# Optimization experiments

Measured on AMD Instinct MI355X. Metric: run time of the kernel, lower is better.

Reference implementation:

```python
import jax, jax.numpy as jnp
import numpy as np

NEG_INF = -1e9  # same masked_fill constant as the torch module
ALPHA = 0.1     # LeakyReLU negative slope


def setup_inputs() -> dict:
    key = jax.random.key(0)
    k1, k2, k3, k4, k5 = jax.random.split(key, 5)
    B, N, Din, Dout = 8, 2048, 512, 512
    features = jax.random.normal(k1, (B, N, Din), dtype=jnp.float32)
    graph = jax.random.randint(k2, (B, N, N), 0, 2, dtype=jnp.int64)
    # xavier_uniform with gain=1.414: limit = gain*sqrt(6/(fan_in+fan_out))
    lim_w = 1.414 * np.sqrt(6.0 / (Din + Dout))
    w = jax.random.uniform(k3, (Din, Dout), jnp.float32, -lim_w, lim_w)
    lim_a = 1.414 * np.sqrt(6.0 / (Dout + 1))
    a1 = jax.random.uniform(k4, (Dout, 1), jnp.float32, -lim_a, lim_a)
    a2 = jax.random.uniform(k5, (Dout, 1), jnp.float32, -lim_a, lim_a)
    return {"features": features, "graph": graph, "w": w, "a1": a1, "a2": a2}


def reference(features, graph, w, a1, a2):
    # hidden: [B, N, Dout]
    hidden = jnp.einsum("bni,io->bno", features, w)
    s1 = hidden @ a1  # [B, N, 1] -> broadcasts over columns
    s2 = hidden @ a2  # [B, N, 1] -> transposed broadcasts over rows
    # e[b,i,j] = leaky_relu(s1[b,i] + s2[b,j])
    e = jax.nn.leaky_relu(s1 + jnp.swapaxes(s2, 1, 2), negative_slope=ALPHA)
    e = jnp.where(graph == 0, NEG_INF, e)
    attn = jax.nn.softmax(e, axis=-1)  # [B, N, N]; dropout p=0 -> identity
    h_prime = jnp.einsum("bij,bjo->bio", attn, hidden)
    return jax.nn.elu(h_prime)  # concat=True
```

## Files before the change

kernel.cpp:

```cpp
#include <hip/hip_runtime.h>
#include <math.h>

#define B_ 8
#define N_ 2048
#define D_ 512
#define NROWS (B_ * N_)
#define NEG_ALPHA 0.1f

typedef __bf16 bf16;
typedef __bf16 bf16x4 __attribute__((ext_vector_type(4)));
typedef __bf16 bf16x8 __attribute__((ext_vector_type(8)));
typedef float f32x4 __attribute__((ext_vector_type(4)));
typedef float f32x16 __attribute__((ext_vector_type(16)));

#define HTB_BATCH ((D_ / 32) * (N_ / 16) * 512)

__global__ __launch_bounds__(256) void k_prep(const float* __restrict__ W,
                                              bf16* __restrict__ Wt) {
  const int dout = blockIdx.x;
  const int t = threadIdx.x;
#pragma unroll
  for (int p = 0; p < 2; ++p) {
    int din = t + p * 256;
    Wt[dout * D_ + din] = (bf16)W[din * D_ + dout];
  }
}

__global__ __launch_bounds__(256) void k_wa(const float* __restrict__ W,
                                            const float* __restrict__ a1,
                                            const float* __restrict__ a2,
                                            float* __restrict__ wa1,
                                            float* __restrict__ wa2) {
  const int wv = threadIdx.x >> 6, lane = threadIdx.x & 63;
  const int row = blockIdx.x * 4 + wv;
  const float* wr = W + (size_t)row * D_;
  float d1 = 0.f, d2 = 0.f;
#pragma unroll
  for (int p = 0; p < 8; ++p) {
    int c = lane + p * 64;
    float w = wr[c];
    d1 = fmaf(w, a1[c], d1);
    d2 = fmaf(w, a2[c], d2);
  }
#pragma unroll
  for (int off = 32; off > 0; off >>= 1) {
    d1 += __shfl_down(d1, off, 64);
    d2 += __shfl_down(d2, off, 64);
  }
  if (lane == 0) {
    wa1[row] = d1;
    wa2[row] = d2;
  }
}

__global__ __launch_bounds__(256) void k_scores_x(const float* __restrict__ X,
                                                  const float* __restrict__ wa1,
                                                  const float* __restrict__ wa2,
                                                  float* __restrict__ s1,
                                                  float* __restrict__ s2) {
  const int wv = threadIdx.x >> 6, lane = threadIdx.x & 63;
  const int r = blockIdx.x * 4 + wv;
  const float* x = X + (size_t)r * D_;
  float d1 = 0.f, d2 = 0.f;
#pragma unroll
  for (int p = 0; p < 2; ++p) {
    int c = lane * 4 + p * 256;
    float4 xv = *(const float4*)&x[c];
    float4 w1 = *(const float4*)&wa1[c];
    float4 w2 = *(const float4*)&wa2[c];
    d1 += xv.x * w1.x + xv.y * w1.y + xv.z * w1.z + xv.w * w1.w;
    d2 += xv.x * w2.x + xv.y * w2.y + xv.z * w2.z + xv.w * w2.w;
  }
#pragma unroll
  for (int off = 32; off > 0; off >>= 1) {
    d1 += __shfl_down(d1, off, 64);
    d2 += __shfl_down(d2, off, 64);
  }
  if (lane == 0) {
    s1[r] = d1;
    s2[r] = d2;
  }
}

#define LDH 40

__global__ __launch_bounds__(256, 2) void k_hiddenT(const float* __restrict__ X,
                                                    const bf16* __restrict__ Wt,
                                                    bf16* __restrict__ HtB) {
  __shared__ bf16 As[128][LDH];
  __shared__ bf16 Bs[128][LDH];
  const int t = threadIdx.x;
  const int m0 = blockIdx.y * 128;
  const int n0 = blockIdx.x * 128;
  const int lane = t & 63, w = t >> 6;
  const int wm = w >> 1, wn = w & 1;
  const int l15 = lane & 15, q = lane >> 4;

  f32x4 acc[4][4];
#pragma unroll
  for (int i = 0; i < 4; ++i)
#pragma unroll
    for (int j = 0; j < 4; ++j) acc[i][j] = (f32x4){0.f, 0.f, 0.f, 0.f};

  bf16x8 av[2];
  float4 bv[4];
#pragma unroll
  for (int p = 0; p < 2; ++p) {
    int s = t + p * 256;
    av[p] = *(const bf16x8*)&Wt[(size_t)(m0 + (s >> 2)) * D_ + (s & 3) * 8];
  }
#pragma unroll
  for (int p = 0; p < 4; ++p) {
    int s = t + p * 256;
    bv[p] = *(const float4*)&X[(size_t)(n0 + (s >> 3)) * D_ + (s & 7) * 4];
  }

  for (int k0 = 0; k0 < D_; k0 += 32) {
    __syncthreads();
#pragma unroll
    for (int p = 0; p < 2; ++p) {
      int s = t + p * 256;
      *(bf16x8*)&As[s >> 2][(s & 3) * 8] = av[p];
    }
#pragma unroll
    for (int p = 0; p < 4; ++p) {
      int s = t + p * 256;
      float4 v = bv[p];
      bf16x4 h = {(bf16)v.x, (bf16)v.y, (bf16)v.z, (bf16)v.w};
      *(bf16x4*)&Bs[s >> 3][(s & 7) * 4] = h;
    }
    __syncthreads();
    if (k0 + 32 < D_) {
#pragma unroll
      for (int p = 0; p < 2; ++p) {
        int s = t + p * 256;
        av[p] = *(const bf16x8*)&Wt[(size_t)(m0 + (s >> 2)) * D_ + k0 + 32 + (s & 3) * 8];
      }
#pragma unroll
      for (int p = 0; p < 4; ++p) {
        int s = t + p * 256;
        bv[p] = *(const float4*)&X[(size_t)(n0 + (s >> 3)) * D_ + k0 + 32 + (s & 7) * 4];
      }
    }
    bf16x8 a[4], bb[4];
#pragma unroll
    for (int i = 0; i < 4; ++i)
      a[i] = *(const bf16x8*)&As[wm * 64 + i * 16 + l15][q * 8];
#pragma unroll
    for (int j = 0; j < 4; ++j)
      bb[j] = *(const bf16x8*)&Bs[wn * 64 + j * 16 + l15][q * 8];
#pragma unroll
    for (int i = 0; i < 4; ++i)
#pragma unroll
      for (int j = 0; j < 4; ++j)
        acc[i][j] =
            __builtin_amdgcn_mfma_f32_16x16x32_bf16(a[i], bb[j], acc[i][j], 0, 0, 0);
  }
#pragma unroll
  for (int i = 0; i < 4; ++i)
#pragma unroll
    for (int r = 0; r < 4; ++r) {
      int dout = m0 + wm * 64 + i * 16 + q * 4 + r;
#pragma unroll
      for (int j = 0; j < 4; ++j) {
        int row = n0 + wn * 64 + j * 16 + l15;
        int bb_ = row >> 11;
        int jj = row & (N_ - 1);
        size_t addr = (size_t)bb_ * HTB_BATCH +
                      ((size_t)((dout >> 5) * (N_ / 16) + (jj >> 4)) * 64 +
                       ((jj >> 3) & 1) * 32 + (dout & 31)) *
                          8 +
                      (jj & 7);
        HtB[addr] = (bf16)acc[i][j][r];
      }
    }
}

#define AT_BM 64
#define AT_BK 64
#define LDP 72
#define NIT (N_ / AT_BK)

#define ATTN_BODY(PS, BC, BN, G0, G1, IT)                                      \
  {                                                                            \
    const int j0_ = (IT)*AT_BK;                                                \
    int gg[8] = {G0.x, G0.y, G0.z, G0.w, G1.x, G1.y, G1.z, G1.w};              \
    {           \
      int itn = (IT) + 2;                                                      \
      int jg = (itn < NIT) ? itn * AT_BK : 0;                                  \
      G0 = *(const int4*)&Gb[(size_t)pi * N_ + jg + pj];                       \
      G1 = *(const int4*)&Gb[(size_t)pi * N_ + jg + pj + 4];                   \
    }                                                                          \
    float pv[8];                                                               \
    {                                                                          \
      f32x4 sA = *(const f32x4*)&s2s[j0_ + pj];                                \
      f32x4 sB = *(const f32x4*)&s2s[j0_ + pj + 4];                            \
      float sv[8] = {sA.x, sA.y, sA.z, sA.w, sB.x, sB.y, sB.z, sB.w};          \
      _Pragma("unroll") for (int q_ = 0; q_ < 8; ++q_) {                       \
        float e = s1r + sv[q_];                                                \
        e = (e > 0.f) ? e : NEG_ALPHA * e;                                     \
        pv[q_] = (gg[q_] != 0) ? __expf(e) : 0.f;                              \
        rsum += pv[q_];                                                        \
      }                                                                        \
    }                                                                          \
    {                                                                          \
      bf16x8 pb = {(bf16)pv[0], (bf16)pv[1], (bf16)pv[2], (bf16)pv[3],         \
                   (bf16)pv[4], (bf16)pv[5], (bf16)pv[6], (bf16)pv[7]};        \
      *(bf16x8*)&Ps[PS][pi][pj] = pb;                                          \
    }                                                                          \
    __syncthreads();            \
    {               \
      int j0n = ((IT) + 1 < NIT) ? ((IT) + 1) * AT_BK : 0;                     \
      _Pragma("unroll") for (int nt = 0; nt < 2; ++nt)                         \
          _Pragma("unroll") for (int ks = 0; ks < 4; ++ks)                     \
              BN[nt][ks] = *(const bf16x8*)&Hb[(size_t)((                      \
                  ((w * 2 + nt) * (N_ / 16) + (j0n >> 4) + ks) * 64 + lane))   \
                  * 8];                                                        \
    }                                                                          \
    _Pragma("unroll") for (int ks = 0; ks < 4; ++ks) {                         \
      const int ko = ks * 16 + hf * 8;                                         \
      bf16x8 a0 = *(const bf16x8*)&Ps[PS][r31][ko];                            \
      bf16x8 a1 = *(const bf16x8*)&Ps[PS][32 + r31][ko];                       \
      acc[0][0] = __builtin_amdgcn_mfma_f32_32x32x16_bf16(a0, BC[0][ks],       \
                                                          acc[0][0], 0, 0, 0); \
      acc[0][1] = __builtin_amdgcn_mfma_f32_32x32x16_bf16(a0, BC[1][ks],       \
                                                          acc[0][1], 0, 0, 0); \
      acc[1][0] = __builtin_amdgcn_mfma_f32_32x32x16_bf16(a1, BC[0][ks],       \
                                                          acc[1][0], 0, 0, 0); \
      acc[1][1] = __builtin_amdgcn_mfma_f32_32x32x16_bf16(a1, BC[1][ks],       \
                                                          acc[1][1], 0, 0, 0); \
    }                                                                          \
  }

__global__ __launch_bounds__(512) void k_attn(const bf16* __restrict__ HtB,
                                              const int* __restrict__ graph,
                                              const float* __restrict__ s1,
                                              const float* __restrict__ s2,
                                              float* __restrict__ out) {
  __shared__ __align__(16) bf16 Ps[2][AT_BM][LDP];
  __shared__ float s2s[N_];
  __shared__ float sum_part[AT_BM][8];
  __shared__ float row_sum[AT_BM];

  const int t = threadIdx.x;
  const int bid = blockIdx.x;
  const int b = bid & 7;
  const int i0 = (bid >> 3) * AT_BM;
  const int lane = t & 63, w = t >> 6;
  const int r31 = lane & 31, hf = lane >> 5;

  const bf16* Hb = HtB + (size_t)b * HTB_BATCH;
  const int* Gb = graph + ((size_t)b * N_ + i0) * N_;

  for (int c = t; c < N_; c += 512) s2s[c] = s2[b * N_ + c];

  const int pi = t >> 3;
  const int pj = (t & 7) * 8;
  const float s1r = s1[b * N_ + i0 + pi];
  float rsum = 0.f;

  f32x16 acc[2][2];
#pragma unroll
  for (int i = 0; i < 2; ++i)
#pragma unroll
    for (int j = 0; j < 2; ++j)
#pragma unroll
      for (int r = 0; r < 16; ++r) acc[i][j][r] = 0.f;

  bf16x8 bA[2][4], bB[2][4];
#pragma unroll
  for (int nt = 0; nt < 2; ++nt)
#pragma unroll
    for (int ks = 0; ks < 4; ++ks)
      bA[nt][ks] = *(const bf16x8*)&Hb[(size_t)(
          ((w * 2 + nt) * (N_ / 16) + ks) * 64 + lane) * 8];
  int4 ga0 = *(const int4*)&Gb[(size_t)pi * N_ + pj];
  int4 ga1 = *(const int4*)&Gb[(size_t)pi * N_ + pj + 4];
  int4 gb0 = *(const int4*)&Gb[(size_t)pi * N_ + AT_BK + pj];
  int4 gb1 = *(const int4*)&Gb[(size_t)pi * N_ + AT_BK + pj + 4];

  __syncthreads();

#pragma unroll 1
  for (int i2 = 0; i2 < NIT / 2; ++i2) {
    const int it0 = i2 * 2;
    ATTN_BODY(0, bA, bB, ga0, ga1, it0);
    ATTN_BODY(1, bB, bA, gb0, gb1, it0 + 1);
  }

  sum_part[pi][t & 7] = rsum;
  __syncthreads();
  if (t < AT_BM) {
    float s = 0.f;
#pragma unroll
    for (int k = 0; k < 8; ++k) s += sum_part[t][k];
    row_sum[t] = s;
  }
  __syncthreads();

#pragma unroll
  for (int mt = 0; mt < 2; ++mt) {
    float inv[16];
#pragma unroll
    for (int r = 0; r < 16; ++r)
      inv[r] = 1.f / row_sum[mt * 32 + (r & 3) + 8 * (r >> 2) + 4 * hf];
#pragma unroll
    for (int nt = 0; nt < 2; ++nt) {
      const int d = w * 64 + nt * 32 + r31;
#pragma unroll
      for (int r = 0; r < 16; ++r) {
        int i = mt * 32 + (r & 3) + 8 * (r >> 2) + 4 * hf;
        float x = acc[mt][nt][r] * inv[r];
        out[((size_t)b * N_ + i0 + i) * D_ + d] = (x > 0.f) ? x : expm1f(x);
      }
    }
  }
}

extern "C" void kernel_launch(void* const* d_in, const int* in_sizes, int n_in,
                              void* d_out, int out_size, void* d_ws,
                              size_t ws_size, hipStream_t stream) {
  const float* X = (const float*)d_in[0];
  const int* graph = (const int*)d_in[1];
  const float* W = (const float*)d_in[2];
  const float* a1 = (const float*)d_in[3];
  const float* a2 = (const float*)d_in[4];
  float* out = (float*)d_out;

  char* ws = (char*)d_ws;
  bf16* Wt = (bf16*)ws;
  bf16* HtB = (bf16*)(ws + (1 << 19));
  float* s1 = (float*)(ws + (1 << 19) + (16 << 20));
  float* s2 = s1 + NROWS;
  float* wa1 = s2 + NROWS;
  float* wa2 = wa1 + D_;

  hipLaunchKernelGGL(k_prep, dim3(512), dim3(256), 0, stream, W, Wt);
  hipLaunchKernelGGL(k_wa, dim3(128), dim3(256), 0, stream, W, a1, a2, wa1, wa2);
  hipLaunchKernelGGL(k_scores_x, dim3(NROWS / 4), dim3(256), 0, stream, X, wa1,
                     wa2, s1, s2);
  hipLaunchKernelGGL(k_hiddenT, dim3(NROWS / 128, D_ / 128), dim3(256), 0,
                     stream, X, Wt, HtB);
  hipLaunchKernelGGL(k_attn, dim3(N_ / AT_BM * B_), dim3(512), 0, stream, HtB,
                     graph, s1, s2, out);
}
```

Measured before the change: 276.6 us.

## Pre-pack adjacency mask to bits and stage it in LDS for attention

```diff
diff --git a/kernel.cpp b/kernel.cpp
--- a/kernel.cpp
+++ b/kernel.cpp
@@ -17,12 +17,22 @@
 
 __global__ __launch_bounds__(256) void k_prep(const float* __restrict__ W,
                                               bf16* __restrict__ Wt) {
-  const int dout = blockIdx.x;
-  const int t = threadIdx.x;
-#pragma unroll
-  for (int p = 0; p < 2; ++p) {
-    int din = t + p * 256;
-    Wt[dout * D_ + din] = (bf16)W[din * D_ + dout];
+  __shared__ float tile[64][65];
+  const int din0 = blockIdx.y * 64, dout0 = blockIdx.x * 64;
+  const int tx = threadIdx.x & 63, tg = threadIdx.x >> 6;
+#pragma unroll
+  for (int rr = 0; rr < 16; ++rr) {
+    int dr = tg * 16 + rr;
+    tile[dr][tx] = W[(size_t)(din0 + dr) * D_ + dout0 + tx];
+  }
+  __syncthreads();
+#pragma unroll
+  for (int rr = 0; rr < 4; ++rr) {
+    int dl = rr * 16 + (threadIdx.x >> 4);
+    int nl = (threadIdx.x & 15) * 4;
+    bf16x4 v = {(bf16)tile[nl][dl], (bf16)tile[nl + 1][dl],
+                (bf16)tile[nl + 2][dl], (bf16)tile[nl + 3][dl]};
+    *(bf16x4*)&Wt[(size_t)(dout0 + dl) * D_ + din0 + nl] = v;
   }
 }
 
@@ -57,7 +67,8 @@
                                                   const float* __restrict__ wa1,
                                                   const float* __restrict__ wa2,
                                                   float* __restrict__ s1,
-                                                  float* __restrict__ s2) {
+                                                  float* __restrict__ s2,
+                                                  bf16* __restrict__ Xb) {
   const int wv = threadIdx.x >> 6, lane = threadIdx.x & 63;
   const int r = blockIdx.x * 4 + wv;
   const float* x = X + (size_t)r * D_;
@@ -70,6 +81,8 @@
     float4 w2 = *(const float4*)&wa2[c];
     d1 += xv.x * w1.x + xv.y * w1.y + xv.z * w1.z + xv.w * w1.w;
     d2 += xv.x * w2.x + xv.y * w2.y + xv.z * w2.z + xv.w * w2.w;
+    bf16x4 h = {(bf16)xv.x, (bf16)xv.y, (bf16)xv.z, (bf16)xv.w};
+    *(bf16x4*)&Xb[(size_t)r * D_ + c] = h;
   }
 #pragma unroll
   for (int off = 32; off > 0; off >>= 1) {
@@ -82,9 +95,25 @@
   }
 }
 
+__global__ __launch_bounds__(256) void k_gpack(const int* __restrict__ G,
+                                               unsigned int* __restrict__ GB) {
+  const size_t g = (size_t)blockIdx.x * 256 + threadIdx.x;
+  const int* src = G + g * 32;
+  unsigned int bits = 0;
+#pragma unroll
+  for (int p = 0; p < 8; ++p) {
+    int4 v = *(const int4*)&src[p * 4];
+    bits |= (unsigned)(v.x != 0) << (p * 4);
+    bits |= (unsigned)(v.y != 0) << (p * 4 + 1);
+    bits |= (unsigned)(v.z != 0) << (p * 4 + 2);
+    bits |= (unsigned)(v.w != 0) << (p * 4 + 3);
+  }
+  GB[g] = bits;
+}
+
 #define LDH 40
 
-__global__ __launch_bounds__(256, 2) void k_hiddenT(const float* __restrict__ X,
+__global__ __launch_bounds__(256, 2) void k_hiddenT(const bf16* __restrict__ Xb,
                                                     const bf16* __restrict__ Wt,
                                                     bf16* __restrict__ HtB) {
   __shared__ bf16 As[128][LDH];
@@ -102,17 +131,12 @@
 #pragma unroll
     for (int j = 0; j < 4; ++j) acc[i][j] = (f32x4){0.f, 0.f, 0.f, 0.f};
 
-  bf16x8 av[2];
-  float4 bv[4];
+  bf16x8 av[2], bv[2];
 #pragma unroll
   for (int p = 0; p < 2; ++p) {
     int s = t + p * 256;
     av[p] = *(const bf16x8*)&Wt[(size_t)(m0 + (s >> 2)) * D_ + (s & 3) * 8];
-  }
-#pragma unroll
-  for (int p = 0; p < 4; ++p) {
-    int s = t + p * 256;
-    bv[p] = *(const float4*)&X[(size_t)(n0 + (s >> 3)) * D_ + (s & 7) * 4];
+    bv[p] = *(const bf16x8*)&Xb[(size_t)(n0 + (s >> 2)) * D_ + (s & 3) * 8];
   }
 
   for (int k0 = 0; k0 < D_; k0 += 32) {
@@ -121,13 +145,7 @@
     for (int p = 0; p < 2; ++p) {
       int s = t + p * 256;
       *(bf16x8*)&As[s >> 2][(s & 3) * 8] = av[p];
-    }
-#pragma unroll
-    for (int p = 0; p < 4; ++p) {
-      int s = t + p * 256;
-      float4 v = bv[p];
-      bf16x4 h = {(bf16)v.x, (bf16)v.y, (bf16)v.z, (bf16)v.w};
-      *(bf16x4*)&Bs[s >> 3][(s & 7) * 4] = h;
+      *(bf16x8*)&Bs[s >> 2][(s & 3) * 8] = bv[p];
     }
     __syncthreads();
     if (k0 + 32 < D_) {
@@ -135,11 +153,7 @@
       for (int p = 0; p < 2; ++p) {
         int s = t + p * 256;
         av[p] = *(const bf16x8*)&Wt[(size_t)(m0 + (s >> 2)) * D_ + k0 + 32 + (s & 3) * 8];
-      }
-#pragma unroll
-      for (int p = 0; p < 4; ++p) {
-        int s = t + p * 256;
-        bv[p] = *(const float4*)&X[(size_t)(n0 + (s >> 3)) * D_ + k0 + 32 + (s & 7) * 4];
+        bv[p] = *(const bf16x8*)&Xb[(size_t)(n0 + (s >> 2)) * D_ + k0 + 32 + (s & 3) * 8];
       }
     }
     bf16x8 a[4], bb[4];
@@ -180,17 +194,12 @@
 #define AT_BK 64
 #define LDP 72
 #define NIT (N_ / AT_BK)
-
-#define ATTN_BODY(PS, BC, BN, G0, G1, IT)                                      \
+#define GROW 272
+
+#define ATTN_BODY(PS, BC, BN, IT)                                              \
   {                                                                            \
     const int j0_ = (IT)*AT_BK;                                                \
-    int gg[8] = {G0.x, G0.y, G0.z, G0.w, G1.x, G1.y, G1.z, G1.w};              \
-    {           \
-      int itn = (IT) + 2;                                                      \
-      int jg = (itn < NIT) ? itn * AT_BK : 0;                                  \
-      G0 = *(const int4*)&Gb[(size_t)pi * N_ + jg + pj];                       \
-      G1 = *(const int4*)&Gb[(size_t)pi * N_ + jg + pj + 4];                   \
-    }                                                                          \
+    unsigned gbyte = gb_s[pi][(IT)*8 + (t & 7)];                               \
     float pv[8];                                                               \
     {                                                                          \
       f32x4 sA = *(const f32x4*)&s2s[j0_ + pj];                                \
@@ -199,7 +208,7 @@
       _Pragma("unroll") for (int q_ = 0; q_ < 8; ++q_) {                       \
         float e = s1r + sv[q_];                                                \
         e = (e > 0.f) ? e : NEG_ALPHA * e;                                     \
-        pv[q_] = (gg[q_] != 0) ? __expf(e) : 0.f;                              \
+        pv[q_] = ((gbyte >> q_) & 1) ? __expf(e) : 0.f;                        \
         rsum += pv[q_];                                                        \
       }                                                                        \
     }                                                                          \
@@ -233,12 +242,13 @@
   }
 
 __global__ __launch_bounds__(512) void k_attn(const bf16* __restrict__ HtB,
-                                              const int* __restrict__ graph,
+                                              const unsigned char* __restrict__ GB,
                                               const float* __restrict__ s1,
                                               const float* __restrict__ s2,
                                               float* __restrict__ out) {
   __shared__ __align__(16) bf16 Ps[2][AT_BM][LDP];
   __shared__ float s2s[N_];
+  __shared__ __align__(16) unsigned char gb_s[AT_BM][GROW];
   __shared__ float sum_part[AT_BM][8];
   __shared__ float row_sum[AT_BM];
 
@@ -250,9 +260,16 @@
   const int r31 = lane & 31, hf = lane >> 5;
 
   const bf16* Hb = HtB + (size_t)b * HTB_BATCH;
-  const int* Gb = graph + ((size_t)b * N_ + i0) * N_;
+  const unsigned char* GBb = GB + ((size_t)b * N_ + i0) * (N_ / 8);
 
   for (int c = t; c < N_; c += 512) s2s[c] = s2[b * N_ + c];
+  {
+    int gr = t >> 3, gc = (t & 7) * 32;
+    int4 w0 = *(const int4*)&GBb[(size_t)gr * (N_ / 8) + gc];
+    int4 w1 = *(const int4*)&GBb[(size_t)gr * (N_ / 8) + gc + 16];
+    *(int4*)&gb_s[gr][gc] = w0;
+    *(int4*)&gb_s[gr][gc + 16] = w1;
+  }
 
   const int pi = t >> 3;
   const int pj = (t & 7) * 8;
@@ -274,18 +291,14 @@
     for (int ks = 0; ks < 4; ++ks)
       bA[nt][ks] = *(const bf16x8*)&Hb[(size_t)(
           ((w * 2 + nt) * (N_ / 16) + ks) * 64 + lane) * 8];
-  int4 ga0 = *(const int4*)&Gb[(size_t)pi * N_ + pj];
-  int4 ga1 = *(const int4*)&Gb[(size_t)pi * N_ + pj + 4];
-  int4 gb0 = *(const int4*)&Gb[(size_t)pi * N_ + AT_BK + pj];
-  int4 gb1 = *(const int4*)&Gb[(size_t)pi * N_ + AT_BK + pj + 4];
 
   __syncthreads();
 
 #pragma unroll 1
   for (int i2 = 0; i2 < NIT / 2; ++i2) {
     const int it0 = i2 * 2;
-    ATTN_BODY(0, bA, bB, ga0, ga1, it0);
-    ATTN_BODY(1, bB, bA, gb0, gb1, it0 + 1);
+    ATTN_BODY(0, bA, bB, it0);
+    ATTN_BODY(1, bB, bA, it0 + 1);
   }
 
   sum_part[pi][t & 7] = rsum;
@@ -330,17 +343,21 @@
   char* ws = (char*)d_ws;
   bf16* Wt = (bf16*)ws;
   bf16* HtB = (bf16*)(ws + (1 << 19));
-  float* s1 = (float*)(ws + (1 << 19) + (16 << 20));
+  bf16* Xb = (bf16*)(ws + (1 << 19) + (16 << 20));
+  unsigned int* GBw = (unsigned int*)(ws + (1 << 19) + (32 << 20));
+  float* s1 = (float*)(ws + (1 << 19) + (37 << 20));
   float* s2 = s1 + NROWS;
   float* wa1 = s2 + NROWS;
   float* wa2 = wa1 + D_;
 
-  hipLaunchKernelGGL(k_prep, dim3(512), dim3(256), 0, stream, W, Wt);
+  hipLaunchKernelGGL(k_prep, dim3(8, 8), dim3(256), 0, stream, W, Wt);
   hipLaunchKernelGGL(k_wa, dim3(128), dim3(256), 0, stream, W, a1, a2, wa1, wa2);
   hipLaunchKernelGGL(k_scores_x, dim3(NROWS / 4), dim3(256), 0, stream, X, wa1,
-                     wa2, s1, s2);
+                     wa2, s1, s2, Xb);
+  hipLaunchKernelGGL(k_gpack, dim3((B_ * N_ * N_) / (256 * 32)), dim3(256), 0,
+                     stream, graph, GBw);
   hipLaunchKernelGGL(k_hiddenT, dim3(NROWS / 128, D_ / 128), dim3(256), 0,
-                     stream, X, Wt, HtB);
+                     stream, Xb, Wt, HtB);
   hipLaunchKernelGGL(k_attn, dim3(N_ / AT_BM * B_), dim3(512), 0, stream, HtB,
-                     graph, s1, s2, out);
-}
+                     (const unsigned char*)GBw, s1, s2, out);
+}
```

Measured after the change: 299.3 us. +8.2%, slower.
